# Optimization experiments

Hardware: AMD Instinct MI355X
Metric: run time of the kernel (lower is better)

Reference implementation:

```python
import jax, jax.numpy as jnp
import numpy as np

STRIDE = (2, 2)
PADDING = (1, 1)
DILATION = (1, 1)
KERNEL = (3, 3)


def _out_hw(h_in, w_in):
    h_out = (h_in + 2 * PADDING[0] - DILATION[0] * (KERNEL[0] - 1) - 1) // STRIDE[0] + 1
    w_out = (w_in + 2 * PADDING[1] - DILATION[1] * (KERNEL[1] - 1) - 1) // STRIDE[1] + 1
    return h_out, w_out


def _stride_permutation(h_out, w_out):
    # Single-shot multiplexing row permutation (mirrors _get_stride_permutation).
    s_h, s_w = STRIDE
    if s_h == 1 and s_w == 1:
        return np.arange(h_out * w_out)
    perm = []
    for si in range(s_h):
        for sj in range(s_w):
            for i in range((h_out + s_h - 1) // s_h):
                ai = i * s_h + si
                if ai >= h_out:
                    continue
                for j in range((w_out + s_w - 1) // s_w):
                    aj = j * s_w + sj
                    if aj >= w_out:
                        continue
                    perm.append(ai * w_out + aj)
    return np.asarray(perm, dtype=np.int32)


def setup_inputs() -> dict:
    key = jax.random.key(0)
    kx, kw, kb = jax.random.split(key, 3)
    x = jax.random.normal(kx, (16, 256, 64, 64), dtype=jnp.float32)
    weight = jax.random.normal(kw, (256, 256, 3, 3), dtype=jnp.float32)
    bias = jax.random.normal(kb, (256,), dtype=jnp.float32)
    return {"x": x, "weight": weight, "bias": bias}


def reference(x, weight, bias):
    # Toeplitz matrix-vector product == grouped strided conv.
    out = jax.lax.conv_general_dilated(
        x, weight,
        window_strides=STRIDE,
        padding=[(PADDING[0], PADDING[0]), (PADDING[1], PADDING[1])],
        rhs_dilation=DILATION,
        dimension_numbers=("NCHW", "OIHW", "NCHW"),
        feature_group_count=1,
    )  # [B, Cout, h_out, w_out]
    b, c, h_out, w_out = out.shape
    perm = jnp.asarray(_stride_permutation(h_out, w_out))
    flat = out.reshape(b, c, h_out * w_out)
    # permuted[new_idx] = flat[perm[new_idx]] (single-shot stride multiplexing)
    permuted = flat[:, :, perm]
    return permuted + bias[None, :, None]
```

## Files before the change

### kernel.cpp

```cpp
#include <hip/hip_runtime.h>
#include <cstdint>

typedef __attribute__((ext_vector_type(8))) __bf16 bf16x8;
typedef __attribute__((ext_vector_type(4))) float f32x4;
typedef __attribute__((ext_vector_type(4))) uint32_t u32x4;

#define NB   16
#define CIN  256
#define COUT 256
#define HP   66
#define WP   66
#define KTOT 2304
#define XPB  (HP*WP*256)
#define XPAD_ELEMS (NB*XPB)

__device__ __forceinline__ uint16_t f2bf(float f) {
  uint32_t u = __builtin_bit_cast(uint32_t, f);
  u = (u + 0x7FFFu + ((u >> 16) & 1u)) >> 16;
  return (uint16_t)u;
}

__global__ void border_kernel(uint16_t* __restrict__ xpad) {
  const int idx = blockIdx.x * 256 + threadIdx.x;
  const int b = idx / 16640;
  const int r = idx - b * 16640;
  uint64_t* base = (uint64_t*)(xpad + (size_t)b * XPB);
  int off;
  if (r < 4224) {
    off = r;
  } else if (r < 8448) {
    off = 274560 + (r - 4224);
  } else if (r < 12544) {
    const int i = r - 8448;
    off = (1 + (i >> 6)) * 4224 + (i & 63);
  } else {
    const int i = r - 12544;
    off = (1 + (i >> 6)) * 4224 + 4160 + (i & 63);
  }
  base[off] = 0;
}

__global__ void xpose_kernel(const float* __restrict__ x, uint16_t* __restrict__ xpad) {
  const int lane = threadIdx.x & 63;
  const int wv = threadIdx.x >> 6;
  const int chalf = blockIdx.x & 1;
  const int h = (blockIdx.x >> 1) & 63;
  const int b = blockIdx.x >> 7;
  const int c0 = chalf * 128 + wv * 32;
  const float* src = x + ((size_t)(b * 256 + c0) * 64 + h) * 64 + lane;
  uint16_t* dst = xpad + ((size_t)(b * HP + h + 1) * WP + lane + 1) * 256 + c0;
  #pragma unroll
  for (int g = 0; g < 4; ++g) {
    u32x4 d;
    #pragma unroll
    for (int k = 0; k < 4; ++k) {
      const float v0 = src[(size_t)(g * 8 + 2 * k + 0) * 4096];
      const float v1 = src[(size_t)(g * 8 + 2 * k + 1) * 4096];
      d[k] = (uint32_t)f2bf(v0) | ((uint32_t)f2bf(v1) << 16);
    }
    *(u32x4*)(dst + g * 8) = d;
  }
}

__global__ void wprep_kernel(const float* __restrict__ w, uint16_t* __restrict__ bw) {
  const int gid = blockIdx.x * 256 + threadIdx.x;
  const int co = gid / 288;
  const int r = gid - co * 288;
  const int tap = r >> 5;
  const int ci0 = (r & 31) * 8;
  u32x4 d;
  #pragma unroll
  for (int k = 0; k < 4; ++k) {
    const float v0 = w[((co * 256 + ci0 + 2 * k + 0) * 9) + tap];
    const float v1 = w[((co * 256 + ci0 + 2 * k + 1) * 9) + tap];
    d[k] = (uint32_t)f2bf(v0) | ((uint32_t)f2bf(v1) << 16);
  }
  *(u32x4*)(bw + co * KTOT + tap * 256 + ci0) = d;
}

__device__ __forceinline__ void gl_lds16(const void* g, void* l) {
  __builtin_amdgcn_global_load_lds(
      (__attribute__((address_space(1))) void*)(uintptr_t)g,
      (__attribute__((address_space(3))) void*)(uint32_t)(uintptr_t)l,
      16, 0, 0);
}

__global__ __launch_bounds__(128, 2) void gemm_kernel(
    const uint16_t* __restrict__ xpad, const uint16_t* __restrict__ bw,
    const float* __restrict__ bias, float* __restrict__ out) {
  __shared__ uint16_t lA[2][128 * 64];
  __shared__ uint16_t lB[2][64 * 64];
  const int tid = threadIdx.x;
  const int wv = tid >> 6, lane = tid & 63;
  const int quad = lane >> 4, l15 = lane & 15, l7 = lane & 7;

  const int xcd = blockIdx.x & 7;
  const int grp = blockIdx.x >> 3;
  const int mtile = (xcd << 4) + (grp >> 2);
  const int ntile = grp & 3;
  const int n0 = ntile * 64;
  const int m0 = mtile * 128;
  const int bidx = m0 >> 10;
  const int q0 = m0 & 1023;

  int a_goff[8];
  #pragma unroll
  for (int t = 0; t < 8; ++t) {
    const int c = t * 128 + tid;
    const int row = c >> 3;
    const int kc = (c & 7) ^ (row & 7);
    const int p = q0 + row;
    const int oh = 2 * ((p >> 4) & 15) + ((p >> 9) & 1);
    const int ow = 2 * (p & 15) + ((p >> 8) & 1);
    a_goff[t] = ((bidx * HP + 2 * oh) * WP + 2 * ow) * 256 + kc * 8;
  }
  int b_goff[4];
  #pragma unroll
  for (int t = 0; t < 4; ++t) {
    const int c = t * 128 + tid;
    const int n = c >> 3;
    const int kc = (c & 7) ^ (n & 7);
    b_goff[t] = (n0 + n) * KTOT + kc * 8;
  }

  int aoff[4][2], boff[4][2];
  #pragma unroll
  for (int r = 0; r < 4; ++r)
    #pragma unroll
    for (int s = 0; s < 2; ++s)
      aoff[r][s] = (wv * 64 + r * 16 + l15) * 128 + (((s * 4 + quad) ^ l7) * 16);
  #pragma unroll
  for (int c = 0; c < 4; ++c)
    #pragma unroll
    for (int s = 0; s < 2; ++s)
      boff[c][s] = (c * 16 + l15) * 128 + (((s * 4 + quad) ^ l7) * 16);

  f32x4 acc[4][4];
  #pragma unroll
  for (int r = 0; r < 4; ++r)
    #pragma unroll
    for (int c = 0; c < 4; ++c)
      acc[r][c] = (f32x4){0.f, 0.f, 0.f, 0.f};

  auto stage = [&](int it, int buf) {
    const int tap = it >> 2;
    const int kh = tap / 3, kw = tap - kh * 3;
    const int ci0 = (it & 3) << 6;
    const uint16_t* aptr = xpad + (kh * WP + kw) * 256 + ci0;
    const uint16_t* bptr = bw + tap * 256 + ci0;
    char* la = (char*)&lA[buf][0];
    char* lb = (char*)&lB[buf][0];
    #pragma unroll
    for (int t = 0; t < 8; ++t)
      gl_lds16(aptr + a_goff[t], la + (t * 128 + wv * 64) * 16);
    #pragma unroll
    for (int t = 0; t < 4; ++t)
      gl_lds16(bptr + b_goff[t], lb + (t * 128 + wv * 64) * 16);
  };

  stage(0, 0);
  int buf = 0;
  for (int it = 0; it < 36; ++it) {
    __syncthreads();
    if (it < 35) stage(it + 1, buf ^ 1);
    const char* la = (const char*)&lA[buf][0];
    const char* lb = (const char*)&lB[buf][0];
    #pragma unroll
    for (int s = 0; s < 2; ++s) {
      bf16x8 af[4], bfr[4];
      #pragma unroll
      for (int r = 0; r < 4; ++r) af[r] = *(const bf16x8*)(la + aoff[r][s]);
      #pragma unroll
      for (int c = 0; c < 4; ++c) bfr[c] = *(const bf16x8*)(lb + boff[c][s]);
      #pragma unroll
      for (int r = 0; r < 4; ++r)
        #pragma unroll
        for (int c = 0; c < 4; ++c)
          acc[r][c] = __builtin_amdgcn_mfma_f32_16x16x32_bf16(af[r], bfr[c], acc[r][c], 0, 0, 0);
    }
    buf ^= 1;
  }

  float* obase = out + (size_t)bidx * (COUT * 1024);
  #pragma unroll
  for (int c = 0; c < 4; ++c) {
    const int co = n0 + c * 16 + l15;
    const float bv = bias[co];
    #pragma unroll
    for (int r = 0; r < 4; ++r) {
      const int q = q0 + wv * 64 + r * 16 + quad * 4;
      f32x4 v = acc[r][c];
      v += bv;
      *(f32x4*)(obase + (size_t)co * 1024 + q) = v;
    }
  }
}

extern "C" void kernel_launch(void* const* d_in, const int* in_sizes, int n_in,
                              void* d_out, int out_size, void* d_ws, size_t ws_size,
                              hipStream_t stream) {
  const float* x    = (const float*)d_in[0];
  const float* w    = (const float*)d_in[1];
  const float* bias = (const float*)d_in[2];
  float* out = (float*)d_out;
  uint16_t* xpad = (uint16_t*)d_ws;
  uint16_t* bwq  = xpad + XPAD_ELEMS;

  border_kernel<<<dim3(1040), dim3(256), 0, stream>>>(xpad);
  xpose_kernel<<<dim3(2048), dim3(256), 0, stream>>>(x, xpad);
  wprep_kernel<<<dim3(288), dim3(256), 0, stream>>>(w, bwq);
  gemm_kernel<<<dim3(512), dim3(128), 0, stream>>>(xpad, bwq, bias, out);
}
```

Baseline: 150.7 us.

## Merge prep kernels into one launch and use four waves per GEMM block

Folds the border-zeroing, input transpose and weight conversion into a single prep kernel dispatched on block index, which saves two kernel launches and their gaps. The GEMM block grows from 2 to 4 waves for the same 128x64 tile, so each wave computes a 32x64 sub-tile and issues half as many global-to-LDS loads. This trades fewer accumulators per wave for more waves to hide latency, at the cost of more LDS B-fragment reads per MFMA and more blocks sharing barriers.

```diff
diff --git a/kernel.cpp b/kernel.cpp
--- a/kernel.cpp
+++ b/kernel.cpp
@@ -20,62 +20,63 @@
   return (uint16_t)u;
 }
 
-__global__ void border_kernel(uint16_t* __restrict__ xpad) {
-  const int idx = blockIdx.x * 256 + threadIdx.x;
-  const int b = idx / 16640;
-  const int r = idx - b * 16640;
-  uint64_t* base = (uint64_t*)(xpad + (size_t)b * XPB);
-  int off;
-  if (r < 4224) {
-    off = r;
-  } else if (r < 8448) {
-    off = 274560 + (r - 4224);
-  } else if (r < 12544) {
-    const int i = r - 8448;
-    off = (1 + (i >> 6)) * 4224 + (i & 63);
+__global__ void prep_kernel(const float* __restrict__ x, const float* __restrict__ w,
+                            uint16_t* __restrict__ xpad, uint16_t* __restrict__ bw) {
+  const int bid = blockIdx.x;
+  const int tid = threadIdx.x;
+  if (bid < 2048) {
+    const int lane = tid & 63;
+    const int wvi = tid >> 6;
+    const int chalf = bid & 1;
+    const int h = (bid >> 1) & 63;
+    const int b = bid >> 7;
+    const int c0 = chalf * 128 + wvi * 32;
+    const float* src = x + ((size_t)(b * 256 + c0) * 64 + h) * 64 + lane;
+    uint16_t* dst = xpad + ((size_t)(b * HP + h + 1) * WP + lane + 1) * 256 + c0;
+    #pragma unroll
+    for (int g = 0; g < 4; ++g) {
+      u32x4 d;
+      #pragma unroll
+      for (int k = 0; k < 4; ++k) {
+        const float v0 = src[(size_t)(g * 8 + 2 * k + 0) * 4096];
+        const float v1 = src[(size_t)(g * 8 + 2 * k + 1) * 4096];
+        d[k] = (uint32_t)f2bf(v0) | ((uint32_t)f2bf(v1) << 16);
+      }
+      *(u32x4*)(dst + g * 8) = d;
+    }
+  } else if (bid < 3088) {
+    const int idx = (bid - 2048) * 256 + tid;
+    const int b = idx / 16640;
+    const int r = idx - b * 16640;
+    uint64_t* base = (uint64_t*)(xpad + (size_t)b * XPB);
+    int off;
+    if (r < 4224) {
+      off = r;
+    } else if (r < 8448) {
+      off = 274560 + (r - 4224);
+    } else if (r < 12544) {
+      const int i = r - 8448;
+      off = (1 + (i >> 6)) * 4224 + (i & 63);
+    } else {
+      const int i = r - 12544;
+      off = (1 + (i >> 6)) * 4224 + 4160 + (i & 63);
+    }
+    base[off] = 0;
   } else {
-    const int i = r - 12544;
-    off = (1 + (i >> 6)) * 4224 + 4160 + (i & 63);
-  }
-  base[off] = 0;
-}
-
-__global__ void xpose_kernel(const float* __restrict__ x, uint16_t* __restrict__ xpad) {
-  const int lane = threadIdx.x & 63;
-  const int wv = threadIdx.x >> 6;
-  const int chalf = blockIdx.x & 1;
-  const int h = (blockIdx.x >> 1) & 63;
-  const int b = blockIdx.x >> 7;
-  const int c0 = chalf * 128 + wv * 32;
-  const float* src = x + ((size_t)(b * 256 + c0) * 64 + h) * 64 + lane;
-  uint16_t* dst = xpad + ((size_t)(b * HP + h + 1) * WP + lane + 1) * 256 + c0;
-  #pragma unroll
-  for (int g = 0; g < 4; ++g) {
+    const int gid = (bid - 3088) * 256 + tid;
+    const int co = gid / 288;
+    const int r = gid - co * 288;
+    const int tap = r >> 5;
+    const int ci0 = (r & 31) * 8;
     u32x4 d;
     #pragma unroll
     for (int k = 0; k < 4; ++k) {
-      const float v0 = src[(size_t)(g * 8 + 2 * k + 0) * 4096];
-      const float v1 = src[(size_t)(g * 8 + 2 * k + 1) * 4096];
+      const float v0 = w[((co * 256 + ci0 + 2 * k + 0) * 9) + tap];
+      const float v1 = w[((co * 256 + ci0 + 2 * k + 1) * 9) + tap];
       d[k] = (uint32_t)f2bf(v0) | ((uint32_t)f2bf(v1) << 16);
     }
-    *(u32x4*)(dst + g * 8) = d;
-  }
-}
-
-__global__ void wprep_kernel(const float* __restrict__ w, uint16_t* __restrict__ bw) {
-  const int gid = blockIdx.x * 256 + threadIdx.x;
-  const int co = gid / 288;
-  const int r = gid - co * 288;
-  const int tap = r >> 5;
-  const int ci0 = (r & 31) * 8;
-  u32x4 d;
-  #pragma unroll
-  for (int k = 0; k < 4; ++k) {
-    const float v0 = w[((co * 256 + ci0 + 2 * k + 0) * 9) + tap];
-    const float v1 = w[((co * 256 + ci0 + 2 * k + 1) * 9) + tap];
-    d[k] = (uint32_t)f2bf(v0) | ((uint32_t)f2bf(v1) << 16);
-  }
-  *(u32x4*)(bw + co * KTOT + tap * 256 + ci0) = d;
+    *(u32x4*)(bw + co * KTOT + tap * 256 + ci0) = d;
+  }
 }
 
 __device__ __forceinline__ void gl_lds16(const void* g, void* l) {
@@ -85,7 +86,7 @@
       16, 0, 0);
 }
 
-__global__ __launch_bounds__(128, 2) void gemm_kernel(
+__global__ __launch_bounds__(256, 2) void gemm_kernel(
     const uint16_t* __restrict__ xpad, const uint16_t* __restrict__ bw,
     const float* __restrict__ bias, float* __restrict__ out) {
   __shared__ uint16_t lA[2][128 * 64];
@@ -103,41 +104,41 @@
   const int bidx = m0 >> 10;
   const int q0 = m0 & 1023;
 
-  int a_goff[8];
-  #pragma unroll
-  for (int t = 0; t < 8; ++t) {
-    const int c = t * 128 + tid;
-    const int row = c >> 3;
-    const int kc = (c & 7) ^ (row & 7);
+  int a_goff[4];
+  #pragma unroll
+  for (int t = 0; t < 4; ++t) {
+    const int slot = t * 256 + tid;
+    const int row = slot >> 3;
+    const int kc = (slot & 7) ^ (row & 7);
     const int p = q0 + row;
     const int oh = 2 * ((p >> 4) & 15) + ((p >> 9) & 1);
     const int ow = 2 * (p & 15) + ((p >> 8) & 1);
     a_goff[t] = ((bidx * HP + 2 * oh) * WP + 2 * ow) * 256 + kc * 8;
   }
-  int b_goff[4];
-  #pragma unroll
-  for (int t = 0; t < 4; ++t) {
-    const int c = t * 128 + tid;
-    const int n = c >> 3;
-    const int kc = (c & 7) ^ (n & 7);
+  int b_goff[2];
+  #pragma unroll
+  for (int t = 0; t < 2; ++t) {
+    const int slot = t * 256 + tid;
+    const int n = slot >> 3;
+    const int kc = (slot & 7) ^ (n & 7);
     b_goff[t] = (n0 + n) * KTOT + kc * 8;
   }
 
-  int aoff[4][2], boff[4][2];
-  #pragma unroll
-  for (int r = 0; r < 4; ++r)
+  int aoff[2][2], boff[4][2];
+  #pragma unroll
+  for (int r = 0; r < 2; ++r)
     #pragma unroll
     for (int s = 0; s < 2; ++s)
-      aoff[r][s] = (wv * 64 + r * 16 + l15) * 128 + (((s * 4 + quad) ^ l7) * 16);
+      aoff[r][s] = (wv * 32 + r * 16 + l15) * 128 + (((s * 4 + quad) ^ l7) * 16);
   #pragma unroll
   for (int c = 0; c < 4; ++c)
     #pragma unroll
     for (int s = 0; s < 2; ++s)
       boff[c][s] = (c * 16 + l15) * 128 + (((s * 4 + quad) ^ l7) * 16);
 
-  f32x4 acc[4][4];
-  #pragma unroll
-  for (int r = 0; r < 4; ++r)
+  f32x4 acc[2][4];
+  #pragma unroll
+  for (int r = 0; r < 2; ++r)
     #pragma unroll
     for (int c = 0; c < 4; ++c)
       acc[r][c] = (f32x4){0.f, 0.f, 0.f, 0.f};
@@ -151,11 +152,11 @@
     char* la = (char*)&lA[buf][0];
     char* lb = (char*)&lB[buf][0];
     #pragma unroll
-    for (int t = 0; t < 8; ++t)
-      gl_lds16(aptr + a_goff[t], la + (t * 128 + wv * 64) * 16);
-    #pragma unroll
     for (int t = 0; t < 4; ++t)
-      gl_lds16(bptr + b_goff[t], lb + (t * 128 + wv * 64) * 16);
+      gl_lds16(aptr + a_goff[t], la + (t * 256 + wv * 64) * 16);
+    #pragma unroll
+    for (int t = 0; t < 2; ++t)
+      gl_lds16(bptr + b_goff[t], lb + (t * 256 + wv * 64) * 16);
   };
 
   stage(0, 0);
@@ -167,13 +168,13 @@
     const char* lb = (const char*)&lB[buf][0];
     #pragma unroll
     for (int s = 0; s < 2; ++s) {
-      bf16x8 af[4], bfr[4];
-      #pragma unroll
-      for (int r = 0; r < 4; ++r) af[r] = *(const bf16x8*)(la + aoff[r][s]);
+      bf16x8 af[2], bfr[4];
+      #pragma unroll
+      for (int r = 0; r < 2; ++r) af[r] = *(const bf16x8*)(la + aoff[r][s]);
       #pragma unroll
       for (int c = 0; c < 4; ++c) bfr[c] = *(const bf16x8*)(lb + boff[c][s]);
       #pragma unroll
-      for (int r = 0; r < 4; ++r)
+      for (int r = 0; r < 2; ++r)
         #pragma unroll
         for (int c = 0; c < 4; ++c)
           acc[r][c] = __builtin_amdgcn_mfma_f32_16x16x32_bf16(af[r], bfr[c], acc[r][c], 0, 0, 0);
@@ -187,8 +188,8 @@
     const int co = n0 + c * 16 + l15;
     const float bv = bias[co];
     #pragma unroll
-    for (int r = 0; r < 4; ++r) {
-      const int q = q0 + wv * 64 + r * 16 + quad * 4;
+    for (int r = 0; r < 2; ++r) {
+      const int q = q0 + wv * 32 + r * 16 + quad * 4;
       f32x4 v = acc[r][c];
       v += bv;
       *(f32x4*)(obase + (size_t)co * 1024 + q) = v;
@@ -206,8 +207,6 @@
   uint16_t* xpad = (uint16_t*)d_ws;
   uint16_t* bwq  = xpad + XPAD_ELEMS;
 
-  border_kernel<<<dim3(1040), dim3(256), 0, stream>>>(xpad);
-  xpose_kernel<<<dim3(2048), dim3(256), 0, stream>>>(x, xpad);
-  wprep_kernel<<<dim3(288), dim3(256), 0, stream>>>(w, bwq);
-  gemm_kernel<<<dim3(512), dim3(128), 0, stream>>>(xpad, bwq, bias, out);
-}
+  prep_kernel<<<dim3(3376), dim3(256), 0, stream>>>(x, w, xpad, bwq);
+  gemm_kernel<<<dim3(512), dim3(256), 0, stream>>>(xpad, bwq, bias, out);
+}
```

After: 138.5 us. 8.1% less time.
